# Kernel tuning notes

Measured on AMD Instinct MI355X. Metric: run time of the kernel, lower is better.

## Reference

```python
import jax, jax.numpy as jnp
import numpy as np
from jax import lax

LENS = 11
R = LENS // 2


def _make_kernels(lens):
    """distance_kernel: euclidean distance of each offset from the window center.
    lens_shape_mask: binary disk (circular aperture) mask inside the lens window."""
    r = lens // 2
    yy, xx = jnp.meshgrid(jnp.arange(lens) - r, jnp.arange(lens) - r, indexing='ij')
    dist = jnp.sqrt((yy * yy + xx * xx).astype(jnp.float32))
    mask = (dist <= (r + 0.5)).astype(jnp.float32)
    return dist, mask


def setup_inputs() -> dict:
    key = jax.random.key(0)
    k1, k2, k3 = jax.random.split(key, 3)
    B, H, W = 4, 1024, 1024
    rgb = jax.random.uniform(k1, (B, 3, H, W), dtype=jnp.float32)
    # relative disparity w.r.t. focal plane (signed, ~[-4, 4])
    disp = jax.random.normal(k2, (B, 1, H, W), dtype=jnp.float32) * 2.0
    x = jnp.concatenate([rgb, disp], axis=1)
    lens_effects = jax.random.uniform(k3, (4, 1), dtype=jnp.float32) * 8.0 + 1.0
    diskernel, lens_mask = _make_kernels(LENS)
    return {"x": x, "lens_effects": lens_effects, "diskernel": diskernel, "lens_mask": lens_mask}


def reference(x, lens_effects, diskernel, lens_mask):
    """Depth-dependent scatter splatting with soft occlusion, expressed as a gather.
    Each source pixel p splats its color onto neighbors within its circle of
    confusion coc(p) = |lens_effect * disp(p)|, weighted by the disk aperture
    mask and a soft edge (clip(coc - dist + 0.5, 0, 1)). Occlusion: sources in
    front of the destination (larger disparity) dominate via a sigmoid gate.
    Scatter-to-q == gather-at-q over all kernel offsets of the padded image."""
    B, C, H, W = x.shape
    disp_dst = x[:, 3:4]
    scale = lens_effects.reshape(B, 1, 1, 1)
    # replication pad (ReplicationPad2d(lens // 2))
    xpad = jnp.pad(x, ((0, 0), (0, 0), (R, R), (R, R)), mode='edge')

    dys, dxs = np.meshgrid(np.arange(LENS), np.arange(LENS), indexing='ij')
    dys = jnp.asarray(dys.reshape(-1), dtype=jnp.int32)
    dxs = jnp.asarray(dxs.reshape(-1), dtype=jnp.int32)
    dvals = diskernel.reshape(-1)
    mvals = lens_mask.reshape(-1)

    def step(carry, inputs):
        num, den = carry
        dy, dx, d, m = inputs
        src = lax.dynamic_slice(xpad, (0, 0, dy, dx), (B, C, H, W))
        src_rgb, src_disp = src[:, :3], src[:, 3:4]
        coc = jnp.abs(scale * src_disp)                    # per-source CoC radius
        w = m * jnp.clip(coc - d + 0.5, 0.0, 1.0)          # soft disk membership
        occ = jax.nn.sigmoid(4.0 * (src_disp - disp_dst))  # front occludes back
        w = w * occ
        return (num + w * src_rgb, den + w), None

    num0 = jnp.zeros((B, 3, H, W), dtype=x.dtype)
    den0 = jnp.zeros((B, 1, H, W), dtype=x.dtype)
    (num, den), _ = lax.scan(step, (num0, den0), (dys, dxs, dvals, mvals))
    return num / (den + 1e-8)
```

## Files before the change

### kernel.cpp

```cpp
#include <hip/hip_runtime.h>

#define LENSZ 11
#define RAD   5
#define TSX   128
#define TSY   16
#define WINX  (TSX + LENSZ - 1)
#define WINY  (TSY + LENSZ - 1)
#define RS    140
#define NPAIR 69
#define IMG_H 1024
#define IMG_W 1024
#define HW    (IMG_H * IMG_W)

#define C4L2  (-5.770780163555854f)
#define DEADC (-3000.0f)

typedef __fp16 v2h __attribute__((ext_vector_type(2)));

__device__ __forceinline__ float dot2acc(float acc, v2h a, v2h b) {
    asm("v_dot2_f32_f16 %0, %1, %2, %0" : "+v"(acc) : "v"(a), "v"(b));
    return acc;
}

constexpr float C0V(int dy, int dx) {
    switch (dy * dy + dx * dx) {
        case 0:  return  0.5f;
        case 1:  return -0.5f;
        case 2:  return -0.914213562f;
        case 4:  return -1.5f;
        case 5:  return -1.736067977f;
        case 8:  return -2.328427125f;
        case 9:  return -2.5f;
        case 10: return -2.662277660f;
        case 13: return -3.105551275f;
        case 16: return -3.5f;
        case 17: return -3.623105626f;
        case 18: return -3.742640687f;
        case 20: return -3.972135955f;
        case 25: return -4.5f;
        case 26: return -4.599019514f;
        case 29: return -4.885164807f;
        default: return DEADC;
    }
}

__shared__ __align__(16) float  dpl[WINY * RS];
__shared__ __align__(8)  __fp16 rpl[WINY * RS];
__shared__ __align__(8)  __fp16 gpl[WINY * RS];
__shared__ __align__(8)  __fp16 bpl[WINY * RS];

template<int ADY, int XMN, int XMX>
__device__ __forceinline__ void do_row(
    int wy, int x8, float scale, const float (&G)[8], v2h one2,
    float (&nr)[8], float (&ng)[8], float (&nb)[8], float (&dn)[8])
{
    const v2h zero2 = {(__fp16)0.f, (__fp16)0.f};
    const v2h onee2 = {(__fp16)1.f, (__fp16)1.f};
#pragma unroll
    for (int kxe = (XMN & ~1); kxe <= XMX + 7; kxe += 2) {
        const int xo = x8 + kxe;
        const float2 d2 = *reinterpret_cast<const float2*>(&dpl[wy * RS + xo]);
        const v2h r2 = *reinterpret_cast<const v2h*>(&rpl[wy * RS + xo]);
        const v2h g2 = *reinterpret_cast<const v2h*>(&gpl[wy * RS + xo]);
        const v2h b2 = *reinterpret_cast<const v2h*>(&bpl[wy * RS + xo]);
        const v2h coc2 = __builtin_amdgcn_cvt_pkrtz(scale * fabsf(d2.x),
                                                    scale * fabsf(d2.y));
        const float Ea = __builtin_amdgcn_exp2f(C4L2 * d2.x);
        const float Eb = __builtin_amdgcn_exp2f(C4L2 * d2.y);
#pragma unroll
        for (int j = 0; j < 8; ++j) {
            const float c0a = C0V(ADY, kxe - j - RAD);
            const float c0b = C0V(ADY, kxe + 1 - j - RAD);
            if (c0a == DEADC && c0b == DEADC) continue;
            const float fa = fmaf(Ea, G[j], 1.f);
            const float fb = fmaf(Eb, G[j], 1.f);
            const float rr = __builtin_amdgcn_rcpf(fa * fb);
            const v2h occ2 = __builtin_amdgcn_cvt_pkrtz(rr * fb, rr * fa);
            const v2h c0h = {(__fp16)c0a, (__fp16)c0b};
            v2h t = coc2 + c0h;
            t = __builtin_elementwise_max(t, zero2);
            t = __builtin_elementwise_min(t, onee2);
            const v2h wh = t * occ2;
            nr[j] = dot2acc(nr[j], wh, r2);
            ng[j] = dot2acc(ng[j], wh, g2);
            nb[j] = dot2acc(nb[j], wh, b2);
            dn[j] = dot2acc(dn[j], wh, one2);
        }
    }
}

__global__ __launch_bounds__(256, 4) void scatter_render_kernel(
    const float* __restrict__ x,
    const float* __restrict__ lens,
    float* __restrict__ out)
{
    const int b   = blockIdx.z;
    const int bx0 = blockIdx.x * TSX;
    const int by0 = blockIdx.y * TSY;
    const int tx  = threadIdx.x;
    const int ty  = threadIdx.y;
    const int tid = ty * 16 + tx;

    const float scale = lens[b];
    const float* xb = x + (size_t)b * 4 * HW;

    for (int p = tid; p < WINY * NPAIR; p += 256) {
        int wy = p / NPAIR;
        int px = (p - wy * NPAIR) * 2;
        int gy = by0 - RAD + wy;  gy = min(max(gy, 0), IMG_H - 1);
        int g0 = bx0 - RAD + px;      g0 = min(max(g0, 0), IMG_W - 1);
        int g1 = bx0 - RAD + px + 1;  g1 = min(max(g1, 0), IMG_W - 1);
        int ba = gy * IMG_W + g0;
        int bb = gy * IMG_W + g1;
        float r0 = xb[ba],          r1 = xb[bb];
        float q0 = xb[ba + HW],     q1 = xb[bb + HW];
        float s0 = xb[ba + 2 * HW], s1 = xb[bb + 2 * HW];
        float d0 = xb[ba + 3 * HW], d1 = xb[bb + 3 * HW];
        int oh = wy * RS + px;
        *reinterpret_cast<v2h*>(&rpl[oh]) = __builtin_amdgcn_cvt_pkrtz(r0, r1);
        *reinterpret_cast<v2h*>(&gpl[oh]) = __builtin_amdgcn_cvt_pkrtz(q0, q1);
        *reinterpret_cast<v2h*>(&bpl[oh]) = __builtin_amdgcn_cvt_pkrtz(s0, s1);
        *reinterpret_cast<float2*>(&dpl[oh]) = make_float2(d0, d1);
    }
    __syncthreads();

    const int x8 = 8 * tx;
    float G[8];
#pragma unroll
    for (int j = 0; j < 8; ++j) {
        float dd = dpl[(ty + RAD) * RS + x8 + j + RAD];
        G[j] = __builtin_amdgcn_exp2f(-C4L2 * dd);
    }
    v2h one2; one2.x = (__fp16)1.f; one2.y = (__fp16)1.f;

    float nr[8] = {0.f, 0.f, 0.f, 0.f, 0.f, 0.f, 0.f, 0.f};
    float ng[8] = {0.f, 0.f, 0.f, 0.f, 0.f, 0.f, 0.f, 0.f};
    float nb[8] = {0.f, 0.f, 0.f, 0.f, 0.f, 0.f, 0.f, 0.f};
    float dn[8] = {0.f, 0.f, 0.f, 0.f, 0.f, 0.f, 0.f, 0.f};

#pragma unroll 1
    for (int t = 0; t < 2; ++t)
        do_row<5, 3, 7>(ty + t * 10, x8, scale, G, one2, nr, ng, nb, dn);
#pragma unroll 1
    for (int t = 0; t < 2; ++t)
        do_row<4, 2, 8>(ty + 1 + t * 8, x8, scale, G, one2, nr, ng, nb, dn);
#pragma unroll 1
    for (int t = 0; t < 2; ++t)
        do_row<3, 1, 9>(ty + 2 + t * 6, x8, scale, G, one2, nr, ng, nb, dn);
#pragma unroll 1
    for (int t = 0; t < 2; ++t)
        do_row<2, 0, 10>(ty + 3 + t * 4, x8, scale, G, one2, nr, ng, nb, dn);
#pragma unroll 1
    for (int t = 0; t < 2; ++t)
        do_row<1, 0, 10>(ty + 4 + t * 2, x8, scale, G, one2, nr, ng, nb, dn);
    do_row<0, 0, 10>(ty + 5, x8, scale, G, one2, nr, ng, nb, dn);

    const size_t obase = (size_t)b * 3 * HW + (size_t)(by0 + ty) * IMG_W + (bx0 + x8);

    float inv[8];
#pragma unroll
    for (int j = 0; j < 8; ++j)
        inv[j] = __builtin_amdgcn_rcpf(dn[j] + 1e-8f);

#pragma unroll
    for (int h = 0; h < 2; ++h) {
        const int o4 = 4 * h;
        float4 o;
        o.x = nr[o4+0]*inv[o4+0]; o.y = nr[o4+1]*inv[o4+1];
        o.z = nr[o4+2]*inv[o4+2]; o.w = nr[o4+3]*inv[o4+3];
        *reinterpret_cast<float4*>(&out[obase + o4]) = o;
        o.x = ng[o4+0]*inv[o4+0]; o.y = ng[o4+1]*inv[o4+1];
        o.z = ng[o4+2]*inv[o4+2]; o.w = ng[o4+3]*inv[o4+3];
        *reinterpret_cast<float4*>(&out[obase + HW + o4]) = o;
        o.x = nb[o4+0]*inv[o4+0]; o.y = nb[o4+1]*inv[o4+1];
        o.z = nb[o4+2]*inv[o4+2]; o.w = nb[o4+3]*inv[o4+3];
        *reinterpret_cast<float4*>(&out[obase + 2 * HW + o4]) = o;
    }
}

extern "C" void kernel_launch(void* const* d_in, const int* in_sizes, int n_in,
                              void* d_out, int out_size, void* d_ws, size_t ws_size,
                              hipStream_t stream) {
    const float* x    = (const float*)d_in[0];
    const float* lens = (const float*)d_in[1];
    float* out        = (float*)d_out;

    const int B = in_sizes[1];

    dim3 block(16, 16, 1);
    dim3 grid(IMG_W / TSX, IMG_H / TSY, B);
    scatter_render_kernel<<<grid, block, 0, stream>>>(x, lens, out);
}
```

Before: 108.6 us.

## Precompute CoC and exp terms in LDS, pack planes into swizzled uint4

Computes the packed half-precision CoC and the sigmoid exponent term once per window pixel during the tile load, rather than once per thread per inner-loop step. The per-pair exp terms are stored as bf16-rounded pairs in a separate LDS array. The four fp16 planes (coc, r, g, b) are interleaved into a single XOR-swizzled uint4 array, so each step does one 128-bit LDS read instead of four scattered reads. This removes redundant exp2 and abs/scale work from the hot loop and cuts LDS instructions. In exchange, the exp terms lose precision to bf16 rounding, and G is now the reciprocal of a rounded value rather than an exact exp2.

```diff
diff --git a/kernel.cpp b/kernel.cpp
--- a/kernel.cpp
+++ b/kernel.cpp
@@ -6,8 +6,9 @@
 #define TSY   16
 #define WINX  (TSX + LENSZ - 1)
 #define WINY  (TSY + LENSZ - 1)
-#define RS    140
 #define NPAIR 69
+#define PKS   70
+#define ESS   70
 #define IMG_H 1024
 #define IMG_W 1024
 #define HW    (IMG_H * IMG_W)
@@ -44,29 +45,29 @@
     }
 }
 
-__shared__ __align__(16) float  dpl[WINY * RS];
-__shared__ __align__(8)  __fp16 rpl[WINY * RS];
-__shared__ __align__(8)  __fp16 gpl[WINY * RS];
-__shared__ __align__(8)  __fp16 bpl[WINY * RS];
+__device__ __forceinline__ int pswz(int s) { return s ^ ((s >> 3) & 7); }
+
+__shared__ __align__(16) uint4    pk[WINY * PKS];
+__shared__ __align__(16) unsigned es[WINY * ESS];
 
 template<int ADY, int XMN, int XMX>
 __device__ __forceinline__ void do_row(
-    int wy, int x8, float scale, const float (&G)[8], v2h one2,
+    int wy, int tx4, const float (&G)[8], v2h one2,
     float (&nr)[8], float (&ng)[8], float (&nb)[8], float (&dn)[8])
 {
     const v2h zero2 = {(__fp16)0.f, (__fp16)0.f};
     const v2h onee2 = {(__fp16)1.f, (__fp16)1.f};
 #pragma unroll
     for (int kxe = (XMN & ~1); kxe <= XMX + 7; kxe += 2) {
-        const int xo = x8 + kxe;
-        const float2 d2 = *reinterpret_cast<const float2*>(&dpl[wy * RS + xo]);
-        const v2h r2 = *reinterpret_cast<const v2h*>(&rpl[wy * RS + xo]);
-        const v2h g2 = *reinterpret_cast<const v2h*>(&gpl[wy * RS + xo]);
-        const v2h b2 = *reinterpret_cast<const v2h*>(&bpl[wy * RS + xo]);
-        const v2h coc2 = __builtin_amdgcn_cvt_pkrtz(scale * fabsf(d2.x),
-                                                    scale * fabsf(d2.y));
-        const float Ea = __builtin_amdgcn_exp2f(C4L2 * d2.x);
-        const float Eb = __builtin_amdgcn_exp2f(C4L2 * d2.y);
+        const int s = tx4 + (kxe >> 1);
+        const uint4 q = pk[wy * PKS + pswz(s)];
+        const v2h coc2 = *reinterpret_cast<const v2h*>(&q.x);
+        const v2h r2   = *reinterpret_cast<const v2h*>(&q.y);
+        const v2h g2   = *reinterpret_cast<const v2h*>(&q.z);
+        const v2h b2   = *reinterpret_cast<const v2h*>(&q.w);
+        const unsigned ue = es[wy * ESS + s];
+        const float Ea = __uint_as_float(ue << 16);
+        const float Eb = __uint_as_float(ue & 0xffff0000u);
 #pragma unroll
         for (int j = 0; j < 8; ++j) {
             const float c0a = C0V(ADY, kxe - j - RAD);
@@ -106,7 +107,8 @@
 
     for (int p = tid; p < WINY * NPAIR; p += 256) {
         int wy = p / NPAIR;
-        int px = (p - wy * NPAIR) * 2;
+        int sl = p - wy * NPAIR;
+        int px = sl * 2;
         int gy = by0 - RAD + wy;  gy = min(max(gy, 0), IMG_H - 1);
         int g0 = bx0 - RAD + px;      g0 = min(max(g0, 0), IMG_W - 1);
         int g1 = bx0 - RAD + px + 1;  g1 = min(max(g1, 0), IMG_W - 1);
@@ -116,11 +118,22 @@
         float q0 = xb[ba + HW],     q1 = xb[bb + HW];
         float s0 = xb[ba + 2 * HW], s1 = xb[bb + 2 * HW];
         float d0 = xb[ba + 3 * HW], d1 = xb[bb + 3 * HW];
-        int oh = wy * RS + px;
-        *reinterpret_cast<v2h*>(&rpl[oh]) = __builtin_amdgcn_cvt_pkrtz(r0, r1);
-        *reinterpret_cast<v2h*>(&gpl[oh]) = __builtin_amdgcn_cvt_pkrtz(q0, q1);
-        *reinterpret_cast<v2h*>(&bpl[oh]) = __builtin_amdgcn_cvt_pkrtz(s0, s1);
-        *reinterpret_cast<float2*>(&dpl[oh]) = make_float2(d0, d1);
+        uint4 q;
+        v2h h;
+        h = __builtin_amdgcn_cvt_pkrtz(scale * fabsf(d0), scale * fabsf(d1));
+        q.x = *reinterpret_cast<unsigned*>(&h);
+        h = __builtin_amdgcn_cvt_pkrtz(r0, r1);
+        q.y = *reinterpret_cast<unsigned*>(&h);
+        h = __builtin_amdgcn_cvt_pkrtz(q0, q1);
+        q.z = *reinterpret_cast<unsigned*>(&h);
+        h = __builtin_amdgcn_cvt_pkrtz(s0, s1);
+        q.w = *reinterpret_cast<unsigned*>(&h);
+        pk[wy * PKS + pswz(sl)] = q;
+        float Ea = __builtin_amdgcn_exp2f(C4L2 * d0);
+        float Eb = __builtin_amdgcn_exp2f(C4L2 * d1);
+        unsigned ua = (__float_as_uint(Ea) + 0x8000u) >> 16;
+        unsigned ub = (__float_as_uint(Eb) + 0x8000u) & 0xffff0000u;
+        es[wy * ESS + sl] = ua | ub;
     }
     __syncthreads();
 
@@ -128,8 +141,11 @@
     float G[8];
 #pragma unroll
     for (int j = 0; j < 8; ++j) {
-        float dd = dpl[(ty + RAD) * RS + x8 + j + RAD];
-        G[j] = __builtin_amdgcn_exp2f(-C4L2 * dd);
+        const int cc = x8 + j + RAD;
+        const unsigned ue = es[(ty + RAD) * ESS + (cc >> 1)];
+        const float esd = (cc & 1) ? __uint_as_float(ue & 0xffff0000u)
+                                   : __uint_as_float(ue << 16);
+        G[j] = __builtin_amdgcn_rcpf(esd);
     }
     v2h one2; one2.x = (__fp16)1.f; one2.y = (__fp16)1.f;
 
@@ -138,22 +154,23 @@
     float nb[8] = {0.f, 0.f, 0.f, 0.f, 0.f, 0.f, 0.f, 0.f};
     float dn[8] = {0.f, 0.f, 0.f, 0.f, 0.f, 0.f, 0.f, 0.f};
 
-#pragma unroll 1
-    for (int t = 0; t < 2; ++t)
-        do_row<5, 3, 7>(ty + t * 10, x8, scale, G, one2, nr, ng, nb, dn);
-#pragma unroll 1
-    for (int t = 0; t < 2; ++t)
-        do_row<4, 2, 8>(ty + 1 + t * 8, x8, scale, G, one2, nr, ng, nb, dn);
-#pragma unroll 1
-    for (int t = 0; t < 2; ++t)
-        do_row<3, 1, 9>(ty + 2 + t * 6, x8, scale, G, one2, nr, ng, nb, dn);
-#pragma unroll 1
-    for (int t = 0; t < 2; ++t)
-        do_row<2, 0, 10>(ty + 3 + t * 4, x8, scale, G, one2, nr, ng, nb, dn);
-#pragma unroll 1
-    for (int t = 0; t < 2; ++t)
-        do_row<1, 0, 10>(ty + 4 + t * 2, x8, scale, G, one2, nr, ng, nb, dn);
-    do_row<0, 0, 10>(ty + 5, x8, scale, G, one2, nr, ng, nb, dn);
+    const int tx4 = 4 * tx;
+#pragma unroll 1
+    for (int t = 0; t < 2; ++t)
+        do_row<5, 3, 7>(ty + t * 10, tx4, G, one2, nr, ng, nb, dn);
+#pragma unroll 1
+    for (int t = 0; t < 2; ++t)
+        do_row<4, 2, 8>(ty + 1 + t * 8, tx4, G, one2, nr, ng, nb, dn);
+#pragma unroll 1
+    for (int t = 0; t < 2; ++t)
+        do_row<3, 1, 9>(ty + 2 + t * 6, tx4, G, one2, nr, ng, nb, dn);
+#pragma unroll 1
+    for (int t = 0; t < 2; ++t)
+        do_row<2, 0, 10>(ty + 3 + t * 4, tx4, G, one2, nr, ng, nb, dn);
+#pragma unroll 1
+    for (int t = 0; t < 2; ++t)
+        do_row<1, 0, 10>(ty + 4 + t * 2, tx4, G, one2, nr, ng, nb, dn);
+    do_row<0, 0, 10>(ty + 5, tx4, G, one2, nr, ng, nb, dn);
 
     const size_t obase = (size_t)b * 3 * HW + (size_t)(by0 + ty) * IMG_W + (bx0 + x8);
 
```

New measurement: 101.1 us. -6.9%, faster.
